# Kernel tuning notes

Hardware: AMD Instinct MI355X
Metric: run time of the kernel (lower is better)

## Reference

```python
import jax, jax.numpy as jnp
import numpy as np

B, Q, D = 4, 8192, 256
L, P = 2, 8
H0 = W0 = 128
H1 = W1 = 64
EPS = 1e-5


def _bilinear_sample(feat, gx, gy):
    """grid_sample bilinear, padding_mode='border', align_corners=False.
    feat: (B, D, H, W); gx, gy: (B, N) in [-1, 1]. Returns (B, N, D)."""
    b, d, h, w = feat.shape
    # unnormalize (align_corners=False)
    x = ((gx + 1.0) * w - 1.0) * 0.5
    y = ((gy + 1.0) * h - 1.0) * 0.5
    # border padding: clamp coords into valid range
    x = jnp.clip(x, 0.0, w - 1.0)
    y = jnp.clip(y, 0.0, h - 1.0)
    x0 = jnp.floor(x)
    y0 = jnp.floor(y)
    wx = x - x0
    wy = y - y0
    x0i = x0.astype(jnp.int32)
    y0i = y0.astype(jnp.int32)
    x1i = jnp.minimum(x0i + 1, w - 1)
    y1i = jnp.minimum(y0i + 1, h - 1)
    fhw = feat.reshape(b, d, h * w)  # (B, D, H*W)

    def gather(iy, ix):
        idx = iy * w + ix  # (B, N)
        return jnp.take_along_axis(fhw, idx[:, None, :], axis=2)  # (B, D, N)

    v00 = gather(y0i, x0i)
    v01 = gather(y0i, x1i)
    v10 = gather(y1i, x0i)
    v11 = gather(y1i, x1i)
    wxb = wx[:, None, :]
    wyb = wy[:, None, :]
    top = v00 * (1.0 - wxb) + v01 * wxb
    bot = v10 * (1.0 - wxb) + v11 * wxb
    out = top * (1.0 - wyb) + bot * wyb  # (B, D, N)
    return out.transpose(0, 2, 1)  # (B, N, D)


def setup_inputs() -> dict:
    key = jax.random.key(0)
    ks = jax.random.split(key, 12)
    s = 0.02
    return {
        "q": jax.random.normal(ks[0], (B, Q, D), jnp.float32),
        "map0": jax.random.normal(ks[1], (B, D, H0, W0), jnp.float32),
        "map1": jax.random.normal(ks[2], (B, D, H1, W1), jnp.float32),
        "base_ref": jax.random.uniform(ks[3], (B, L, 2), jnp.float32),
        "Wrd": jax.random.normal(ks[4], (D, L * 2), jnp.float32) * s,
        "brd": jax.random.normal(ks[5], (L * 2,), jnp.float32) * s,
        "Woff": jax.random.normal(ks[6], (D, L * P * 2), jnp.float32) * s,
        "boff": jax.random.normal(ks[7], (L * P * 2,), jnp.float32) * 1.5,
        "Wattn": jax.random.normal(ks[8], (D, L * P), jnp.float32) * s,
        "battn": jax.random.normal(ks[9], (L * P,), jnp.float32) * s,
        "Wout": jax.random.normal(ks[10], (D, D), jnp.float32) * s,
        "bout": jax.random.normal(ks[11], (D,), jnp.float32) * s,
    }


def reference(q, map0, map1, base_ref, Wrd, brd, Woff, boff, Wattn, battn, Wout, bout):
    b, qn, d = q.shape
    maps = [map0, map1]
    # per-level reference points, refined through inverse-sigmoid space
    base = jnp.clip(base_ref, EPS, 1.0 - EPS)[:, None, :, :]  # (B, 1, L, 2)
    logit_base = jnp.log(base / (1.0 - base))
    ref_delta = (q @ Wrd + brd).reshape(b, qn, L, 2)
    ref = jax.nn.sigmoid(logit_base + ref_delta)  # (B, Q, L, 2)
    offsets = (q @ Woff + boff).reshape(b, qn, L, P, 2)
    attn_logits = (q @ Wattn + battn).reshape(b, qn, L * P)
    attn = jax.nn.softmax(attn_logits, axis=-1).reshape(b, qn, L, P)

    out = jnp.zeros((b, qn, d), jnp.float32)
    for level, feat in enumerate(maps):
        h, w = feat.shape[2], feat.shape[3]
        normalizer = jnp.array([w, h], jnp.float32)
        loc = ref[:, :, level, None, :] + offsets[:, :, level] / normalizer  # (B,Q,P,2)
        if level == 1:
            loc = jnp.stack([loc[..., 0], jnp.remainder(loc[..., 1], 1.0)], axis=-1)
        loc = loc * 2.0 - 1.0
        gx = loc[..., 0].reshape(b, qn * P)
        gy = loc[..., 1].reshape(b, qn * P)
        samp = _bilinear_sample(feat, gx, gy).reshape(b, qn, P, d)
        out = out + jnp.sum(samp * attn[:, :, level, :, None], axis=2)
    return out @ Wout + bout
```

## Files before the change

kernel.cpp:

```cpp
#include <hip/hip_runtime.h>
#include <hip/hip_bf16.h>

#define BQ 4
#define QN 8192
#define DD 256
#define LL 2
#define H0c 128
#define W0c 128
#define H1c 64
#define W1c 64
#define EPSF 1e-5f

typedef unsigned short ushort_t;
typedef __attribute__((ext_vector_type(8))) short short8;
typedef __attribute__((ext_vector_type(8))) unsigned short ushortx8;
typedef __attribute__((ext_vector_type(4))) unsigned short ushortx4;
typedef __attribute__((ext_vector_type(4))) float floatx4;
typedef __attribute__((ext_vector_type(4))) _Float16 half4;

static __device__ __forceinline__ unsigned short f2bf(float f) {
    __hip_bfloat16 h = __float2bfloat16(f);
    return __builtin_bit_cast(unsigned short, h);
}
static __device__ __forceinline__ unsigned short f2h(float f) {
    _Float16 h = (_Float16)f;
    return __builtin_bit_cast(unsigned short, h);
}
static __device__ __forceinline__ float h_lo(unsigned int u) {
    _Float16 h = __builtin_bit_cast(_Float16, (unsigned short)(u & 0xffffu));
    return (float)h;
}
static __device__ __forceinline__ float h_hi(unsigned int u) {
    _Float16 h = __builtin_bit_cast(_Float16, (unsigned short)(u >> 16));
    return (float)h;
}

#define PT0 4096
#define PT1 1024
#define PTW 16
__global__ __launch_bounds__(256) void prep(const float* __restrict__ map0, const float* __restrict__ map1,
                                            const float* __restrict__ Wout,
                                            const float* __restrict__ Wrd, const float* __restrict__ brd,
                                            const float* __restrict__ Woff, const float* __restrict__ boff,
                                            const float* __restrict__ Wattn, const float* __restrict__ battn,
                                            ushort_t* __restrict__ mapT0, ushort_t* __restrict__ mapT1,
                                            __hip_bfloat16* __restrict__ WoutT,
                                            float* __restrict__ Wall, float* __restrict__ bias64) {
    __shared__ float tile[64][65];
    int blk = blockIdx.x;
    int tid = threadIdx.x;
    const float* in; ushort_t* outp; int HW, b, c0, hw0; bool tohalf;
    if (blk < PT0) {
        int l = blk; b = l >> 10; int r = l & 1023;
        c0 = (r >> 8) << 6; hw0 = (r & 255) << 6;
        in = map0; outp = mapT0; HW = H0c * W0c; tohalf = true;
    } else if (blk < PT0 + PT1) {
        int l = blk - PT0; b = l >> 8; int r = l & 255;
        c0 = (r >> 6) << 6; hw0 = (r & 63) << 6;
        in = map1; outp = mapT1; HW = H1c * W1c; tohalf = true;
    } else if (blk < PT0 + PT1 + PTW) {
        int l = blk - PT0 - PT1; b = 0;
        c0 = (l >> 2) << 6; hw0 = (l & 3) << 6;
        in = Wout; outp = (ushort_t*)WoutT; HW = DD; tohalf = false;
    } else {
        int l = blk - PT0 - PT1 - PTW;
        int idx = l * 256 + tid;
        int k = idx >> 6, c = idx & 63;
        float v = (c < 4)  ? Wrd[k * 4 + c]
                : (c < 36) ? Woff[k * 32 + (c - 4)]
                : (c < 52) ? Wattn[k * 16 + (c - 36)]
                : 0.f;
        Wall[idx] = v;
        if (idx < 64) {
            float bv = (idx < 4)  ? brd[idx]
                     : (idx < 36) ? boff[idx - 4]
                     : (idx < 52) ? battn[idx - 36]
                     : 0.f;
            bias64[idx] = bv;
        }
        return;
    }
    const float* inb = in + (size_t)b * DD * HW + (size_t)c0 * HW + hw0;
    ushort_t* outb = outp + (size_t)b * DD * HW + (size_t)hw0 * DD + c0;

    int row = tid >> 2;
    int q16 = (tid & 3) * 16;
#pragma unroll
    for (int j = 0; j < 4; j++) {
        float4 v = *(const float4*)(inb + (size_t)row * HW + q16 + j * 4);
        tile[row][q16 + j * 4 + 0] = v.x;
        tile[row][q16 + j * 4 + 1] = v.y;
        tile[row][q16 + j * 4 + 2] = v.z;
        tile[row][q16 + j * 4 + 3] = v.w;
    }
    __syncthreads();

    int hwr = tid >> 4;
    int c4 = (tid & 15) * 4;
#pragma unroll
    for (int jj = 0; jj < 4; jj++) {
        int rr = hwr + jj * 16;
        ushortx4 o;
        if (tohalf) {
            o[0] = f2h(tile[c4 + 0][rr]);
            o[1] = f2h(tile[c4 + 1][rr]);
            o[2] = f2h(tile[c4 + 2][rr]);
            o[3] = f2h(tile[c4 + 3][rr]);
        } else {
            o[0] = f2bf(tile[c4 + 0][rr]);
            o[1] = f2bf(tile[c4 + 1][rr]);
            o[2] = f2bf(tile[c4 + 2][rr]);
            o[3] = f2bf(tile[c4 + 3][rr]);
        }
        *(ushortx4*)(outb + (size_t)rr * DD + c4) = o;
    }
}

__global__ __launch_bounds__(256) void proj_desc(const float* __restrict__ q,
                                                 const float* __restrict__ Wall,
                                                 const float* __restrict__ bias64,
                                                 const float* __restrict__ base_ref,
                                                 int2* __restrict__ dsi,
                                                 half4* __restrict__ dsw) {
    __shared__ float As[32][68];
    __shared__ float Bs[32][64];
    __shared__ float prs[64][68];
    int tid = threadIdx.x;
    int tx = tid & 15, ty = tid >> 4;
    int m0 = blockIdx.x * 64;
    float acc[4][4] = {};

    for (int kt = 0; kt < DD; kt += 32) {
#pragma unroll
        for (int j = 0; j < 8; j++) {
            int e = tid + 256 * j;
            int r = e >> 5, k = e & 31;
            As[k][r] = q[(size_t)(m0 + r) * DD + kt + k];
        }
#pragma unroll
        for (int j = 0; j < 8; j++) {
            int e = tid + 256 * j;
            int k = e >> 6, nn = e & 63;
            Bs[k][nn] = Wall[(size_t)(kt + k) * 64 + nn];
        }
        __syncthreads();
#pragma unroll
        for (int k = 0; k < 32; k++) {
            const float4 a4 = *(const float4*)&As[k][ty * 4];
            const float4 b4 = *(const float4*)&Bs[k][tx * 4];
            acc[0][0] += a4.x * b4.x; acc[0][1] += a4.x * b4.y; acc[0][2] += a4.x * b4.z; acc[0][3] += a4.x * b4.w;
            acc[1][0] += a4.y * b4.x; acc[1][1] += a4.y * b4.y; acc[1][2] += a4.y * b4.z; acc[1][3] += a4.y * b4.w;
            acc[2][0] += a4.z * b4.x; acc[2][1] += a4.z * b4.y; acc[2][2] += a4.z * b4.z; acc[2][3] += a4.z * b4.w;
            acc[3][0] += a4.w * b4.x; acc[3][1] += a4.w * b4.y; acc[3][2] += a4.w * b4.z; acc[3][3] += a4.w * b4.w;
        }
        __syncthreads();
    }

    float4 bias = *(const float4*)&bias64[tx * 4];
#pragma unroll
    for (int i = 0; i < 4; i++) {
        float4 v;
        v.x = acc[i][0] + bias.x;
        v.y = acc[i][1] + bias.y;
        v.z = acc[i][2] + bias.z;
        v.w = acc[i][3] + bias.w;
        *(float4*)&prs[ty * 4 + i][tx * 4] = v;
    }
    __syncthreads();

    int ql = tid >> 2, sq = tid & 3;
    int n = m0 + ql, b = n >> 13;
    const float* p = prs[ql];

    float mx = p[36];
#pragma unroll
    for (int i = 1; i < 16; i++) mx = fmaxf(mx, p[36 + i]);
    float sum = 0.f;
#pragma unroll
    for (int i = 0; i < 16; i++) sum += __expf(p[36 + i] - mx);
    float inv = 1.f / sum;

#pragma unroll
    for (int u = 0; u < 4; u++) {
        int s = sq * 4 + u;
        int l = s >> 3;
        float a = __expf(p[36 + s] - mx) * inv;

        int W = l ? W1c : W0c;
        int H = l ? H1c : H0c;
        float Wf = (float)W, Hf = (float)H;

        float bx = base_ref[(b * LL + l) * 2 + 0];
        float by = base_ref[(b * LL + l) * 2 + 1];
        bx = fminf(fmaxf(bx, EPSF), 1.f - EPSF);
        by = fminf(fmaxf(by, EPSF), 1.f - EPSF);
        float lgx = logf(bx / (1.f - bx));
        float lgy = logf(by / (1.f - by));
        float refx = 1.f / (1.f + __expf(-(lgx + p[l * 2 + 0])));
        float refy = 1.f / (1.f + __expf(-(lgy + p[l * 2 + 1])));

        float locx = refx + p[4 + s * 2 + 0] / Wf;
        float locy = refy + p[4 + s * 2 + 1] / Hf;
        if (l == 1) locy = locy - floorf(locy);

        float gx = locx * 2.f - 1.f;
        float gy = locy * 2.f - 1.f;
        float x = ((gx + 1.f) * Wf - 1.f) * 0.5f;
        float y = ((gy + 1.f) * Hf - 1.f) * 0.5f;
        x = fminf(fmaxf(x, 0.f), Wf - 1.f);
        y = fminf(fmaxf(y, 0.f), Hf - 1.f);
        float x0f = floorf(x), y0f = floorf(y);
        float wx = x - x0f, wy = y - y0f;
        int x0 = (int)x0f, y0 = (int)y0f;
        unsigned int dx = (x0 + 1 <= W - 1) ? DD : 0;
        unsigned int dy = (y0 + 1 <= H - 1) ? (unsigned)(W * DD) : 0;
        int base = ((b * H + y0) * W + x0) * DD;

        float omx = 1.f - wx, omy = 1.f - wy;
        half4 w;
        w[0] = (_Float16)(a * omx * omy);
        w[1] = (_Float16)(a * wx  * omy);
        w[2] = (_Float16)(a * omx * wy);
        w[3] = (_Float16)(a * wx  * wy);

        dsi[(size_t)n * 16 + s] = make_int2(base, (int)((dy << 16) | dx));
        dsw[(size_t)n * 16 + s] = w;
    }
}

__global__ __launch_bounds__(256, 3) void sample_kernel(const ushort_t* __restrict__ mapT0,
                                                        const ushort_t* __restrict__ mapT1,
                                                        const int2* __restrict__ dsi,
                                                        const half4* __restrict__ dsw,
                                                        ushort_t* __restrict__ S,
                                                        int blk0) {
    int tid = threadIdx.x;
    int lx = tid & 63;
    int n = (blockIdx.x + blk0) * 8 + (tid >> 6) * 2 + (lx >> 5);
    int c8 = (lx & 31) * 8;
    const int2*  gi = dsi + (size_t)n * 16;
    const half4* gw = dsw + (size_t)n * 16;

    int2 g[16]; half4 wh[16];
#pragma unroll
    for (int s = 0; s < 16; s++) { g[s] = gi[s]; wh[s] = gw[s]; }

    float acc[8];
#pragma unroll
    for (int i = 0; i < 8; i++) acc[i] = 0.f;

#pragma unroll
    for (int grp = 0; grp < 4; grp++) {
        const ushort_t* mp = (grp < 2) ? mapT0 : mapT1;
        uint4 u[4][4];
#pragma unroll
        for (int j = 0; j < 4; j++) {
            int s = grp * 4 + j;
            int dx = g[s].y & 0xffff;
            int dy = (int)(((unsigned int)g[s].y) >> 16);
            const ushort_t* p0 = mp + g[s].x + c8;
            u[j][0] = *(const uint4*)(p0);
            u[j][1] = *(const uint4*)(p0 + dx);
            u[j][2] = *(const uint4*)(p0 + dy);
            u[j][3] = *(const uint4*)(p0 + dx + dy);
        }
#pragma unroll
        for (int j = 0; j < 4; j++) {
            int s = grp * 4 + j;
            float w0 = (float)wh[s][0], w1 = (float)wh[s][1], w2 = (float)wh[s][2], w3 = (float)wh[s][3];
#pragma unroll
            for (int corner = 0; corner < 4; corner++) {
                uint4 v = u[j][corner];
                float wc = (corner == 0) ? w0 : (corner == 1) ? w1 : (corner == 2) ? w2 : w3;
                acc[0] += wc * h_lo(v.x); acc[1] += wc * h_hi(v.x);
                acc[2] += wc * h_lo(v.y); acc[3] += wc * h_hi(v.y);
                acc[4] += wc * h_lo(v.z); acc[5] += wc * h_hi(v.z);
                acc[6] += wc * h_lo(v.w); acc[7] += wc * h_hi(v.w);
            }
        }
    }
    ushortx8 o;
#pragma unroll
    for (int i = 0; i < 8; i++) o[i] = f2bf(acc[i]);
    *(ushortx8*)(S + (size_t)n * DD + c8) = o;
}

__global__ __launch_bounds__(256) void out_mfma(const ushort_t* __restrict__ S,
                                                const ushort_t* __restrict__ WT,
                                                const float* __restrict__ bout,
                                                float* __restrict__ out) {
    __shared__ ushort_t wlds[64][256];
    int tid = threadIdx.x;
    int n0c = blockIdx.x * 64;
    int wave = tid >> 6, lane = tid & 63;
    int m0 = blockIdx.y * 64 + wave * 16;
    int mrow = lane & 15, quad = lane >> 4;

#pragma unroll
    for (int i = 0; i < 8; i++) {
        int idx = tid + 256 * i;
        int row = idx >> 5, c = idx & 31;
        *(uint4*)&wlds[row][(c ^ (row & 31)) * 8] =
            *(const uint4*)(WT + (size_t)(n0c + row) * DD + c * 8);
    }
    __syncthreads();

    const ushort_t* Sp = S + (size_t)(m0 + mrow) * DD + quad * 8;
    short8 a[8];
#pragma unroll
    for (int k = 0; k < 8; k++) a[k] = *(const short8*)(Sp + k * 32);

    floatx4 acc[4];
#pragma unroll
    for (int nt = 0; nt < 4; nt++) acc[nt] = {0.f, 0.f, 0.f, 0.f};

#pragma unroll
    for (int nt = 0; nt < 4; nt++) {
        int row = nt * 16 + mrow;
#pragma unroll
        for (int k = 0; k < 8; k++) {
            int c = k * 4 + quad;
            short8 b = *(const short8*)&wlds[row][(c ^ (row & 31)) * 8];
            acc[nt] = __builtin_amdgcn_mfma_f32_16x16x32_bf16(a[k], b, acc[nt], 0, 0, 0);
        }
    }

    int rbase = quad * 4;
#pragma unroll
    for (int nt = 0; nt < 4; nt++) {
        float bv = bout[n0c + nt * 16 + mrow];
#pragma unroll
        for (int r = 0; r < 4; r++) {
            out[(size_t)(m0 + rbase + r) * DD + n0c + nt * 16 + mrow] = acc[nt][r] + bv;
        }
    }
}

extern "C" void kernel_launch(void* const* d_in, const int* in_sizes, int n_in,
                              void* d_out, int out_size, void* d_ws, size_t ws_size,
                              hipStream_t stream) {
    const float* q        = (const float*)d_in[0];
    const float* map0     = (const float*)d_in[1];
    const float* map1     = (const float*)d_in[2];
    const float* base_ref = (const float*)d_in[3];
    const float* Wrd      = (const float*)d_in[4];
    const float* brd      = (const float*)d_in[5];
    const float* Woff     = (const float*)d_in[6];
    const float* boff     = (const float*)d_in[7];
    const float* Wattn    = (const float*)d_in[8];
    const float* battn    = (const float*)d_in[9];
    const float* Wout     = (const float*)d_in[10];
    const float* bout     = (const float*)d_in[11];
    float* out = (float*)d_out;

    char* ws = (char*)d_ws;
    ushort_t*       mapT0  = (ushort_t*)(ws + 0);
    ushort_t*       mapT1  = (ushort_t*)(ws + 33554432);
    __hip_bfloat16* WoutT  = (__hip_bfloat16*)(ws + 41943040);
    float*          Wall   = (float*)(ws + 42074112);
    float*          bias64 = (float*)(ws + 42139648);
    int2*           dsi    = (int2*)(ws + 42139904);
    half4*          dsw    = (half4*)(ws + 46334208);
    ushort_t*       Sbuf   = (ushort_t*)(ws + 50528512);

    prep<<<dim3(PT0 + PT1 + PTW + 64), dim3(256), 0, stream>>>(
        map0, map1, Wout, Wrd, brd, Woff, boff, Wattn, battn,
        mapT0, mapT1, WoutT, Wall, bias64);

    proj_desc<<<dim3(BQ * QN / 64), dim3(256), 0, stream>>>(q, Wall, bias64, base_ref, dsi, dsw);

    sample_kernel<<<dim3(BQ * QN / 16), dim3(256), 0, stream>>>(
        mapT0, mapT1, dsi, dsw, Sbuf, 0);
    sample_kernel<<<dim3(BQ * QN / 16), dim3(256), 0, stream>>>(
        mapT0, mapT1, dsi, dsw, Sbuf, BQ * QN / 16);

    out_mfma<<<dim3(4, BQ * QN / 64), dim3(256), 0, stream>>>(
        Sbuf, (const ushort_t*)WoutT, bout, out);
}
```

Baseline: 248.1 us.

## Fuse bilinear sampling with output projection MFMA in one kernel

Merges the sampling kernel and the output-projection GEMM into a single kernel. Each block samples 8 queries, stages the bf16 results in LDS (zero-padded to 16 rows), and runs MFMA against Wout read straight from global memory, writing fp32 output with bias. This removes the intermediate S buffer round trip and two extra launches. In exchange, half of each MFMA tile is wasted on padding and every block re-reads the full Wout from global/L2 instead of using an LDS-staged tile.

```diff
diff --git a/kernel.cpp b/kernel.cpp
--- a/kernel.cpp
+++ b/kernel.cpp
@@ -228,15 +228,20 @@
     }
 }
 
-__global__ __launch_bounds__(256, 3) void sample_kernel(const ushort_t* __restrict__ mapT0,
-                                                        const ushort_t* __restrict__ mapT1,
-                                                        const int2* __restrict__ dsi,
-                                                        const half4* __restrict__ dsw,
-                                                        ushort_t* __restrict__ S,
-                                                        int blk0) {
+__global__ __launch_bounds__(256, 3) void sample_out(const ushort_t* __restrict__ mapT0,
+                                                     const ushort_t* __restrict__ mapT1,
+                                                     const int2* __restrict__ dsi,
+                                                     const half4* __restrict__ dsw,
+                                                     const ushort_t* __restrict__ WT,
+                                                     const float* __restrict__ bout,
+                                                     float* __restrict__ out) {
+    __shared__ ushort_t slds[16][256];
     int tid = threadIdx.x;
     int lx = tid & 63;
-    int n = (blockIdx.x + blk0) * 8 + (tid >> 6) * 2 + (lx >> 5);
+    int wave = tid >> 6;
+    int ql = wave * 2 + (lx >> 5);
+    int nbase = blockIdx.x * 8;
+    int n = nbase + ql;
     int c8 = (lx & 31) * 8;
     const int2*  gi = dsi + (size_t)n * 16;
     const half4* gw = dsw + (size_t)n * 16;
@@ -279,59 +284,52 @@
             }
         }
     }
+
     ushortx8 o;
 #pragma unroll
     for (int i = 0; i < 8; i++) o[i] = f2bf(acc[i]);
-    *(ushortx8*)(S + (size_t)n * DD + c8) = o;
-}
-
-__global__ __launch_bounds__(256) void out_mfma(const ushort_t* __restrict__ S,
-                                                const ushort_t* __restrict__ WT,
-                                                const float* __restrict__ bout,
-                                                float* __restrict__ out) {
-    __shared__ ushort_t wlds[64][256];
-    int tid = threadIdx.x;
-    int n0c = blockIdx.x * 64;
-    int wave = tid >> 6, lane = tid & 63;
-    int m0 = blockIdx.y * 64 + wave * 16;
-    int mrow = lane & 15, quad = lane >> 4;
-
-#pragma unroll
-    for (int i = 0; i < 8; i++) {
-        int idx = tid + 256 * i;
-        int row = idx >> 5, c = idx & 31;
-        *(uint4*)&wlds[row][(c ^ (row & 31)) * 8] =
-            *(const uint4*)(WT + (size_t)(n0c + row) * DD + c * 8);
+    {
+        int chunk = (lx & 31);
+        *(ushortx8*)&slds[ql][((chunk ^ ql) & 31) * 8] = o;
+        int zr = 8 + (tid >> 5);
+        ushortx8 z = {0, 0, 0, 0, 0, 0, 0, 0};
+        *(ushortx8*)&slds[zr][(((tid & 31) ^ zr) & 31) * 8] = z;
     }
     __syncthreads();
 
-    const ushort_t* Sp = S + (size_t)(m0 + mrow) * DD + quad * 8;
+    int mrow = lx & 15, quad = lx >> 4;
+    int j0 = wave * 64;
+
     short8 a[8];
 #pragma unroll
-    for (int k = 0; k < 8; k++) a[k] = *(const short8*)(Sp + k * 32);
-
-    floatx4 acc[4];
-#pragma unroll
-    for (int nt = 0; nt < 4; nt++) acc[nt] = {0.f, 0.f, 0.f, 0.f};
+    for (int k = 0; k < 8; k++) {
+        int chunk = (quad + 4 * k) ^ mrow;
+        a[k] = *(const short8*)&slds[mrow][(chunk & 31) * 8];
+    }
+
+    floatx4 oacc[4];
+#pragma unroll
+    for (int nt = 0; nt < 4; nt++) oacc[nt] = {0.f, 0.f, 0.f, 0.f};
 
 #pragma unroll
     for (int nt = 0; nt < 4; nt++) {
-        int row = nt * 16 + mrow;
+        const ushort_t* Wp = WT + (size_t)(j0 + nt * 16 + mrow) * DD + quad * 8;
 #pragma unroll
         for (int k = 0; k < 8; k++) {
-            int c = k * 4 + quad;
-            short8 b = *(const short8*)&wlds[row][(c ^ (row & 31)) * 8];
-            acc[nt] = __builtin_amdgcn_mfma_f32_16x16x32_bf16(a[k], b, acc[nt], 0, 0, 0);
-        }
-    }
-
-    int rbase = quad * 4;
-#pragma unroll
-    for (int nt = 0; nt < 4; nt++) {
-        float bv = bout[n0c + nt * 16 + mrow];
-#pragma unroll
-        for (int r = 0; r < 4; r++) {
-            out[(size_t)(m0 + rbase + r) * DD + n0c + nt * 16 + mrow] = acc[nt][r] + bv;
+            short8 b = *(const short8*)(Wp + k * 32);
+            oacc[nt] = __builtin_amdgcn_mfma_f32_16x16x32_bf16(a[k], b, oacc[nt], 0, 0, 0);
+        }
+    }
+
+    if (quad < 2) {
+        int rbase = quad * 4;
+#pragma unroll
+        for (int nt = 0; nt < 4; nt++) {
+            float bv = bout[j0 + nt * 16 + mrow];
+#pragma unroll
+            for (int r = 0; r < 4; r++) {
+                out[(size_t)(nbase + rbase + r) * DD + j0 + nt * 16 + mrow] = oacc[nt][r] + bv;
+            }
         }
     }
 }
@@ -361,7 +359,6 @@
     float*          bias64 = (float*)(ws + 42139648);
     int2*           dsi    = (int2*)(ws + 42139904);
     half4*          dsw    = (half4*)(ws + 46334208);
-    ushort_t*       Sbuf   = (ushort_t*)(ws + 50528512);
 
     prep<<<dim3(PT0 + PT1 + PTW + 64), dim3(256), 0, stream>>>(
         map0, map1, Wout, Wrd, brd, Woff, boff, Wattn, battn,
@@ -369,11 +366,6 @@
 
     proj_desc<<<dim3(BQ * QN / 64), dim3(256), 0, stream>>>(q, Wall, bias64, base_ref, dsi, dsw);
 
-    sample_kernel<<<dim3(BQ * QN / 16), dim3(256), 0, stream>>>(
-        mapT0, mapT1, dsi, dsw, Sbuf, 0);
-    sample_kernel<<<dim3(BQ * QN / 16), dim3(256), 0, stream>>>(
-        mapT0, mapT1, dsi, dsw, Sbuf, BQ * QN / 16);
-
-    out_mfma<<<dim3(4, BQ * QN / 64), dim3(256), 0, stream>>>(
-        Sbuf, (const ushort_t*)WoutT, bout, out);
-}
+    sample_out<<<dim3(BQ * QN / 8), dim3(256), 0, stream>>>(
+        mapT0, mapT1, dsi, dsw, (const ushort_t*)WoutT, bout, out);
+}
```

Result: slower. 280.1 us (+12.9%).
